# Kernel tuning notes

Hardware: AMD Instinct MI355X
Metric: run time of the kernel (lower is better)

The kernel has to match this reference:

```python
import jax, jax.numpy as jnp
import numpy as np

N_NODES_PER_GRAPH = 64
NUM_GRAPHS = 2048
N = NUM_GRAPHS * N_NODES_PER_GRAPH  # 131072 total nodes
E = N * 8                           # 1048576 edges
IN_DIM, H1, H2 = 64, 128, 64
OUT_DIM = (N_NODES_PER_GRAPH * N_NODES_PER_GRAPH - N_NODES_PER_GRAPH) // 2  # 2016


def setup_inputs() -> dict:
    key = jax.random.key(0)
    ks = jax.random.split(key, 16)
    s = 0.05
    x = jax.random.normal(ks[0], (N, IN_DIM), dtype=jnp.float32)
    # edges within each graph: offsets within graph + graph base offset
    src_local = jax.random.randint(ks[1], (E,), 0, N_NODES_PER_GRAPH)
    dst_local = jax.random.randint(ks[2], (E,), 0, N_NODES_PER_GRAPH)
    gid = jnp.repeat(jnp.arange(NUM_GRAPHS), E // NUM_GRAPHS) * N_NODES_PER_GRAPH
    edge_index = jnp.stack([src_local + gid, dst_local + gid]).astype(jnp.int64)
    batch = jnp.repeat(jnp.arange(NUM_GRAPHS), N_NODES_PER_GRAPH).astype(jnp.int64)
    eps = jax.random.normal(ks[3], (NUM_GRAPHS, H2), dtype=jnp.float32)
    return {
        "x": x, "edge_index": edge_index, "batch": batch, "eps": eps,
        "w1_rel": jax.random.normal(ks[4], (IN_DIM, H1)) * s,
        "b1": jnp.zeros((H1,), jnp.float32),
        "w1_root": jax.random.normal(ks[5], (IN_DIM, H1)) * s,
        "w2_rel": jax.random.normal(ks[6], (H1, H2)) * s,
        "b2": jnp.zeros((H2,), jnp.float32),
        "w2_root": jax.random.normal(ks[7], (H1, H2)) * s,
        "w3_rel": jax.random.normal(ks[8], (H1, H2)) * s,
        "b3": jnp.zeros((H2,), jnp.float32),
        "w3_root": jax.random.normal(ks[9], (H1, H2)) * s,
        "fc1_w": jax.random.normal(ks[10], (H2, H1)) * s,
        "fc1_b": jnp.zeros((H1,), jnp.float32),
        "fc2_w": jax.random.normal(ks[11], (H1, OUT_DIM)) * s,
        "fc2_b": jnp.zeros((OUT_DIM,), jnp.float32),
    }


def _graph_conv(h, src, dst, w_rel, b, w_root):
    # PyG GraphConv: out_i = W_rel @ (sum_{j in N(i)} h_j) + b + W_root @ h_i
    agg = jax.ops.segment_sum(h[src], dst, num_segments=N)  # [N, d_in]
    return agg @ w_rel + b + h @ w_root


def _segment_mean(h, seg):
    s = jax.ops.segment_sum(h, seg, num_segments=NUM_GRAPHS)
    cnt = jax.ops.segment_sum(jnp.ones((h.shape[0],), h.dtype), seg, num_segments=NUM_GRAPHS)
    return s / jnp.maximum(cnt, 1.0)[:, None]


def reference(x, edge_index, batch, eps, w1_rel, b1, w1_root, w2_rel, b2, w2_root,
              w3_rel, b3, w3_root, fc1_w, fc1_b, fc2_w, fc2_b):
    src, dst = edge_index[0], edge_index[1]
    # encode (dropout p=0.0 -> identity)
    h1 = jax.nn.relu(_graph_conv(x, src, dst, w1_rel, b1, w1_root))
    mu = _segment_mean(_graph_conv(h1, src, dst, w2_rel, b2, w2_root), batch)
    logvar = _segment_mean(_graph_conv(h1, src, dst, w3_rel, b3, w3_root), batch)
    # reparameterize with provided eps
    z = mu + eps * jnp.exp(0.5 * logvar)
    # decode
    h = jax.nn.relu(z @ fc1_w + fc1_b)
    recon = jax.nn.sigmoid(h @ fc2_w + fc2_b)
    return recon, mu, logvar
```

## Files before the change

### kernel.cpp

```cpp
#include <hip/hip_runtime.h>
#include <math.h>

#define NG 2048
#define NPG 64
#define EPG 512
#define ETOT (NG*EPG)
#define IND 64
#define H1D 128
#define H2D 64
#define OUTD 2016

typedef __attribute__((ext_vector_type(8))) short bf16x8;
typedef __attribute__((ext_vector_type(4))) float f32x4;
typedef __attribute__((ext_vector_type(8))) unsigned short u16x8;
typedef __attribute__((ext_vector_type(4))) short s16x4;

__device__ inline short f2b(float f) {
  union { float f; unsigned u; } v; v.f = f;
  unsigned r = (v.u + 0x7FFFu + ((v.u >> 16) & 1u)) >> 16;
  return (short)r;
}

__global__ void p_w1(const float* __restrict__ w1_rel, const float* __restrict__ w1_root,
                     short* __restrict__ WTgF,
                     const float* __restrict__ w2_rel, const float* __restrict__ w2_root,
                     const float* __restrict__ w3_rel, const float* __restrict__ w3_root,
                     const float* __restrict__ fc1_w,
                     short* __restrict__ W23T, short* __restrict__ fc1T) {
  __shared__ float L[4224];
  const int b = blockIdx.x;
  const int tid = threadIdx.x;
  if (b < 8) {
    const int ct = b;
    const int ks = tid >> 6, l = tid & 63;
    const int col = ct*16 + (l & 15);
    const int kb  = ks*32 + (l >> 4)*8;
    short tmp[8];
    #pragma unroll
    for (int j = 0; j < 8; ++j) {
      const int k = kb + j;
      float v = (k < 64) ? w1_rel[k*H1D + col] : w1_root[(k - 64)*H1D + col];
      tmp[j] = f2b(v);
    }
    *(uint4*)&WTgF[(size_t)((ct*4 + ks)*64 + l)*8] = *(uint4*)tmp;
  } else if (b < 12) {
    const int cc = b - 8;
    const int j0 = cc*32;
    const float* wrel  = (cc < 2) ? w2_rel  : w3_rel;
    const float* wroot = (cc < 2) ? w2_root : w3_root;
    const int jl = j0 & 63;
    const int c = tid >> 3, k0 = (tid & 7)*32;
    for (int i = tid; i < 4096; i += 256) {
      int k = i >> 5, cc2 = i & 31;
      L[k*33 + cc2] = wrel[k*H2D + jl + cc2];
    }
    __syncthreads();
    if (k0 < 128)
      for (int kk = 0; kk < 32; ++kk)
        W23T[(size_t)(j0 + c)*264 + k0 + kk] = f2b(L[(k0 + kk)*33 + c]);
    __syncthreads();
    for (int i = tid; i < 4096; i += 256) {
      int k = i >> 5, cc2 = i & 31;
      L[k*33 + cc2] = wroot[k*H2D + jl + cc2];
    }
    __syncthreads();
    if (k0 >= 128)
      for (int kk = 0; kk < 32; ++kk)
        W23T[(size_t)(j0 + c)*264 + k0 + kk] = f2b(L[(k0 + kk - 128)*33 + c]);
  } else {
    const int c0 = (b - 12)*64;
    for (int i = tid; i < 4096; i += 256) {
      int k = i >> 6, c = i & 63;
      L[k*65 + c] = fc1_w[k*H1D + c0 + c];
    }
    __syncthreads();
    const int c = tid >> 2, k0 = (tid & 3)*16;
    for (int kk = 0; kk < 16; ++kk)
      fc1T[(size_t)(c0 + c)*72 + k0 + kk] = f2b(L[(k0 + kk)*65 + c]);
  }
}

__global__ __launch_bounds__(256, 5) void k1_enc(
    const float* __restrict__ x, const int* __restrict__ ei,
    const short* __restrict__ WTgF, const float* __restrict__ b1,
    short* __restrict__ SVb,
    const float* __restrict__ fc2_w, short* __restrict__ WF2g)
{
  __shared__ __align__(16) char smem[31744];
  const int g = blockIdx.x;
  const int tid = threadIdx.x;

  if (g >= NG) {
    float* L = (float*)smem;
    const int bid = g - NG;
    const int c0 = bid*32;
    for (int i = tid; i < 4096; i += 256) {
      int k = i >> 5, c = i & 31;
      L[k*33 + c] = fc2_w[(size_t)k*OUTD + c0 + c];
    }
    __syncthreads();
    const int tl = tid >> 7;
    const int r  = tid & 127;
    const int ks = r >> 5;
    const int lp = r & 31;
    const int ct = bid*2 + tl;
    #pragma unroll
    for (int u = 0; u < 2; ++u) {
      const int l = lp*2 + u;
      const int cl = tl*16 + (l & 15);
      const int kb = ks*32 + (l >> 4)*8;
      short tmp[8];
      #pragma unroll
      for (int j = 0; j < 8; ++j) tmp[j] = f2b(L[(kb + j)*33 + cl]);
      *(uint4*)&WF2g[(size_t)((ct*4 + ks)*64 + l)*8] = *(uint4*)tmp;
    }
    return;
  }

  short* Xb   = (short*)smem;
  short* XbT  = (short*)(smem + 9216);
  short* Ab   = (short*)(smem + 18432);
  unsigned* Au32 = (unsigned*)(smem + 27648);

  const int w = tid >> 6, l = tid & 63;

  const int e0 = g*EPG + tid*2;
  const int2 sp = *(const int2*)&ei[e0];
  const int2 dp = *(const int2*)&ei[ETOT + e0];
  const int s0 = sp.x & 63, d0 = dp.x & 63;
  const int s1 = sp.y & 63, d1 = dp.y & 63;
  const int n = tid & 63, f0 = (tid >> 6) * 16;
  const float* xr = x + (size_t)g*(NPG*IND) + n*IND + f0;
  float4 v0 = *(const float4*)&xr[0];
  float4 v1 = *(const float4*)&xr[4];
  float4 v2 = *(const float4*)&xr[8];
  float4 v3 = *(const float4*)&xr[12];

  for (int i = tid; i < 64*16; i += 256) Au32[i] = 0u;
  __syncthreads();

  atomicAdd(&Au32[d0*16 + (s0 >> 2)], 1u << (8*(s0 & 3)));
  atomicAdd(&Au32[d1*16 + (s1 >> 2)], 1u << (8*(s1 & 3)));

  {
    u16x8 lo, hi;
    lo[0]=(unsigned short)f2b(v0.x); lo[1]=(unsigned short)f2b(v0.y);
    lo[2]=(unsigned short)f2b(v0.z); lo[3]=(unsigned short)f2b(v0.w);
    lo[4]=(unsigned short)f2b(v1.x); lo[5]=(unsigned short)f2b(v1.y);
    lo[6]=(unsigned short)f2b(v1.z); lo[7]=(unsigned short)f2b(v1.w);
    hi[0]=(unsigned short)f2b(v2.x); hi[1]=(unsigned short)f2b(v2.y);
    hi[2]=(unsigned short)f2b(v2.z); hi[3]=(unsigned short)f2b(v2.w);
    hi[4]=(unsigned short)f2b(v3.x); hi[5]=(unsigned short)f2b(v3.y);
    hi[6]=(unsigned short)f2b(v3.z); hi[7]=(unsigned short)f2b(v3.w);
    *(u16x8*)&Xb[n*72 + f0]     = lo;
    *(u16x8*)&Xb[n*72 + f0 + 8] = hi;
    #pragma unroll
    for (int j = 0; j < 8; ++j) {
      XbT[(f0 + j)*72 + n]     = (short)lo[j];
      XbT[(f0 + 8 + j)*72 + n] = (short)hi[j];
    }
  }
  __syncthreads();

  {
    const int row = tid >> 2, qw = tid & 3;
    unsigned wds[4];
    #pragma unroll
    for (int q = 0; q < 4; ++q) wds[q] = Au32[row*16 + qw*4 + q];
    auto pk = [](unsigned wv, int p) -> unsigned {
      unsigned c0 = (wv >> (16*p)) & 255u, c1 = (wv >> (16*p + 8)) & 255u;
      return (unsigned)(unsigned short)f2b((float)c0)
           | ((unsigned)(unsigned short)f2b((float)c1) << 16);
    };
    uint4 oA = { pk(wds[0],0), pk(wds[0],1), pk(wds[1],0), pk(wds[1],1) };
    uint4 oB = { pk(wds[2],0), pk(wds[2],1), pk(wds[3],0), pk(wds[3],1) };
    unsigned* abp = (unsigned*)&Ab[row*72 + qw*16];
    *(uint4*)&abp[0] = oA;
    *(uint4*)&abp[4] = oB;
  }

  {
    const int squad = tid >> 4;
    const int db = (tid & 15) * 4;
    unsigned ps = 0;
    #pragma unroll
    for (int i = 0; i < 4; ++i) ps += Au32[(db + i)*16 + squad];
    ps += __shfl_xor(ps, 1); ps += __shfl_xor(ps, 2);
    ps += __shfl_xor(ps, 4); ps += __shfl_xor(ps, 8);
    if ((tid & 15) == 0) {
      #pragma unroll
      for (int i = 0; i < 4; ++i)
        *(float*)&Ab[(squad*4 + i)*72 + 64] = (float)((ps >> (8*i)) & 255u);
    }
  }

  const int rm = w*16;
  const int fr = l & 15;
  const int koff = (l >> 4) * 8;

  f32x4 agc[4];
  #pragma unroll
  for (int t = 0; t < 4; ++t) agc[t] = (f32x4){0.f,0.f,0.f,0.f};
  #pragma unroll
  for (int ks = 0; ks < 2; ++ks) {
    bf16x8 badj = *(const bf16x8*)&Ab[(rm + fr)*72 + ks*32 + koff];
    #pragma unroll
    for (int t = 0; t < 4; ++t) {
      bf16x8 axt = *(const bf16x8*)&XbT[(t*16 + fr)*72 + ks*32 + koff];
      agc[t] = __builtin_amdgcn_mfma_f32_16x16x32_bf16(axt, badj, agc[t], 0, 0, 0);
    }
  }

  bf16x8 bfr[2][4];
  #pragma unroll
  for (int ct2 = 0; ct2 < 2; ++ct2)
    #pragma unroll
    for (int ks = 0; ks < 4; ++ks)
      bfr[ct2][ks] = *(const bf16x8*)&WTgF[(size_t)(((2*w + ct2)*4 + ks)*64 + l)*8];

  short* AGb = Ab;
  #pragma unroll
  for (int t = 0; t < 4; ++t) {
    s16x4 vv;
    #pragma unroll
    for (int r = 0; r < 4; ++r) vv[r] = f2b(agc[t][r]);
    *(s16x4*)&AGb[(rm + (l & 15))*72 + t*16 + (l >> 4)*4] = vv;
  }

  __syncthreads();

  const float bb0 = b1[(2*w)*16 + fr];
  const float bb1 = b1[(2*w + 1)*16 + fr];
  float hs0 = 0.f, ws0 = 0.f, hs1 = 0.f, ws1 = 0.f;
  #pragma unroll
  for (int rt = 0; rt < 4; ++rt) {
    bf16x8 afr[4];
    #pragma unroll
    for (int ks = 0; ks < 4; ++ks)
      afr[ks] = (ks < 2)
        ? *(const bf16x8*)&AGb[(rt*16 + fr)*72 + ks*32 + koff]
        : *(const bf16x8*)&Xb[(rt*16 + fr)*72 + (ks - 2)*32 + koff];
    f32x4 a0 = (f32x4){0.f,0.f,0.f,0.f}, a1 = (f32x4){0.f,0.f,0.f,0.f};
    #pragma unroll
    for (int ks = 0; ks < 4; ++ks) {
      a0 = __builtin_amdgcn_mfma_f32_16x16x32_bf16(afr[ks], bfr[0][ks], a0, 0, 0, 0);
      a1 = __builtin_amdgcn_mfma_f32_16x16x32_bf16(afr[ks], bfr[1][ks], a1, 0, 0, 0);
    }
    #pragma unroll
    for (int r = 0; r < 4; ++r) {
      const float dgr = *(const float*)&Ab[(rt*16 + (l>>4)*4 + r)*72 + 64];
      float va = fmaxf(a0[r] + bb0, 0.f);
      float vb = fmaxf(a1[r] + bb1, 0.f);
      hs0 += va; ws0 += dgr*va;
      hs1 += vb; ws1 += dgr*vb;
    }
  }
  hs0 += __shfl_down(hs0, 32); ws0 += __shfl_down(ws0, 32);
  hs1 += __shfl_down(hs1, 32); ws1 += __shfl_down(ws1, 32);
  hs0 += __shfl_down(hs0, 16); ws0 += __shfl_down(ws0, 16);
  hs1 += __shfl_down(hs1, 16); ws1 += __shfl_down(ws1, 16);
  if (l < 16) {
    short* svg = SVb + (size_t)g*256;
    svg[(2*w)*16 + l]           = f2b(ws0);
    svg[(2*w + 1)*16 + l]       = f2b(ws1);
    svg[128 + (2*w)*16 + l]     = f2b(hs0);
    svg[128 + (2*w + 1)*16 + l] = f2b(hs1);
  }
}

__global__ __launch_bounds__(256) void k1b_latent(
    const short* __restrict__ SVb, const short* __restrict__ W23T,
    const float* __restrict__ b2, const float* __restrict__ b3,
    const float* __restrict__ eps, const short* __restrict__ fc1T,
    const float* __restrict__ fc1_b,
    float* __restrict__ out_mu, float* __restrict__ out_lv, short* __restrict__ hbufF)
{
  __shared__ short SV[32*264];
  __shared__ short Zt[32*72];
  const int g0 = blockIdx.x * 32;
  const int tid = threadIdx.x;
  const int w = tid >> 6, l = tid & 63;
  const int s = w >> 1;
  const int h = w & 1;
  const int fr = l & 15;
  const int koff = (l >> 4) * 8;

  for (int i = tid; i < 32*64; i += 256) {
    const int r = i >> 6, kq = (i & 63)*4;
    *(s16x4*)&SV[r*264 + kq] = *(const s16x4*)&SVb[(size_t)(g0 + r)*256 + kq];
  }
  __syncthreads();

  f32x4 acc[4];
  #pragma unroll
  for (int t = 0; t < 4; ++t) acc[t] = (f32x4){0.f,0.f,0.f,0.f};
  #pragma unroll
  for (int ks = 0; ks < 8; ++ks) {
    bf16x8 a = *(const bf16x8*)&SV[(s*16 + fr)*264 + ks*32 + koff];
    #pragma unroll
    for (int j = 0; j < 2; ++j) {
      bf16x8 bm = *(const bf16x8*)&W23T[((2*h + j)*16 + fr)*264 + ks*32 + koff];
      bf16x8 bl = *(const bf16x8*)&W23T[((2*h + j + 4)*16 + fr)*264 + ks*32 + koff];
      acc[j]     = __builtin_amdgcn_mfma_f32_16x16x32_bf16(bm, a, acc[j], 0, 0, 0);
      acc[2 + j] = __builtin_amdgcn_mfma_f32_16x16x32_bf16(bl, a, acc[2 + j], 0, 0, 0);
    }
  }
  {
    const int grow = s*16 + (l & 15);
    const size_t gg = (size_t)(g0 + grow);
    #pragma unroll
    for (int j = 0; j < 2; ++j) {
      const int c0 = (2*h + j)*16 + (l >> 4)*4;
      const float4 bb2 = *(const float4*)&b2[c0];
      const float4 bb3 = *(const float4*)&b3[c0];
      const float4 ev  = *(const float4*)&eps[gg*64 + c0];
      float4 mu, lv;
      mu.x = acc[j][0]*(1.f/64.f) + bb2.x;  lv.x = acc[2+j][0]*(1.f/64.f) + bb3.x;
      mu.y = acc[j][1]*(1.f/64.f) + bb2.y;  lv.y = acc[2+j][1]*(1.f/64.f) + bb3.y;
      mu.z = acc[j][2]*(1.f/64.f) + bb2.z;  lv.z = acc[2+j][2]*(1.f/64.f) + bb3.z;
      mu.w = acc[j][3]*(1.f/64.f) + bb2.w;  lv.w = acc[2+j][3]*(1.f/64.f) + bb3.w;
      *(float4*)&out_mu[gg*64 + c0] = mu;
      *(float4*)&out_lv[gg*64 + c0] = lv;
      s16x4 zs;
      zs[0] = f2b(mu.x + ev.x * __expf(0.5f*lv.x));
      zs[1] = f2b(mu.y + ev.y * __expf(0.5f*lv.y));
      zs[2] = f2b(mu.z + ev.z * __expf(0.5f*lv.z));
      zs[3] = f2b(mu.w + ev.w * __expf(0.5f*lv.w));
      *(s16x4*)&Zt[grow*72 + c0] = zs;
    }
  }
  __syncthreads();

  f32x4 hacc[4];
  #pragma unroll
  for (int t = 0; t < 4; ++t) hacc[t] = (f32x4){0.f,0.f,0.f,0.f};
  #pragma unroll
  for (int ks = 0; ks < 2; ++ks) {
    bf16x8 a = *(const bf16x8*)&Zt[(s*16 + fr)*72 + ks*32 + koff];
    #pragma unroll
    for (int j = 0; j < 4; ++j) {
      bf16x8 b = *(const bf16x8*)&fc1T[((h*4 + j)*16 + fr)*72 + ks*32 + koff];
      hacc[j] = __builtin_amdgcn_mfma_f32_16x16x32_bf16(b, a, hacc[j], 0, 0, 0);
    }
  }
  {
    const int row = s*16 + (l & 15);
    const int rt2 = blockIdx.x*2 + (row >> 4);
    #pragma unroll
    for (int j = 0; j < 4; ++j) {
      const int c0 = (h*4 + j)*16 + (l >> 4)*4;
      const float4 bb = *(const float4*)&fc1_b[c0];
      s16x4 hv;
      hv[0] = f2b(fmaxf(hacc[j][0] + bb.x, 0.f));
      hv[1] = f2b(fmaxf(hacc[j][1] + bb.y, 0.f));
      hv[2] = f2b(fmaxf(hacc[j][2] + bb.z, 0.f));
      hv[3] = f2b(fmaxf(hacc[j][3] + bb.w, 0.f));
      const int ks2 = c0 >> 5;
      const int q   = (c0 >> 3) & 3;
      const int j8  = c0 & 7;
      const int lane = (row & 15) + 16*q;
      *(s16x4*)&hbufF[(size_t)((rt2*4 + ks2)*64 + lane)*8 + j8] = hv;
    }
  }
}

__global__ __launch_bounds__(256, 8) void k2_decoder(
    const short* __restrict__ hbufF, const short* __restrict__ WF2g,
    const float* __restrict__ fc2_b, float* __restrict__ recon)
{
  const int bx = blockIdx.x, by = blockIdx.y;
  const int tid = threadIdx.x;
  const int w = tid >> 6, l = tid & 63;
  const int rt = bx*4 + w;

  bf16x8 ah[4];
  #pragma unroll
  for (int ks = 0; ks < 4; ++ks)
    ah[ks] = *(const bf16x8*)&hbufF[(size_t)((rt*4 + ks)*64 + l)*8];

  f32x4 acc[6];
  #pragma unroll
  for (int t = 0; t < 6; ++t) acc[t] = (f32x4){0.f,0.f,0.f,0.f};

  #pragma unroll
  for (int ks = 0; ks < 4; ++ks) {
    #pragma unroll
    for (int t = 0; t < 6; ++t) {
      const int ct = by*6 + t;
      bf16x8 bw = *(const bf16x8*)&WF2g[(size_t)((ct*4 + ks)*64 + l)*8];
      acc[t] = __builtin_amdgcn_mfma_f32_16x16x32_bf16(bw, ah[ks], acc[t], 0, 0, 0);
    }
  }

  const int row = bx*64 + w*16 + (l & 15);
  #pragma unroll
  for (int t = 0; t < 6; ++t) {
    const int colq = (by*6 + t)*16 + (l >> 4)*4;
    const float4 bb = *(const float4*)&fc2_b[colq];
    float4 o;
    o.x = 1.f/(1.f + __expf(-(acc[t][0] + bb.x)));
    o.y = 1.f/(1.f + __expf(-(acc[t][1] + bb.y)));
    o.z = 1.f/(1.f + __expf(-(acc[t][2] + bb.z)));
    o.w = 1.f/(1.f + __expf(-(acc[t][3] + bb.w)));
    *(float4*)&recon[(size_t)row*OUTD + colq] = o;
  }
}

extern "C" void kernel_launch(void* const* d_in, const int* in_sizes, int n_in,
                              void* d_out, int out_size, void* d_ws, size_t ws_size,
                              hipStream_t stream) {
  const float* x       = (const float*)d_in[0];
  const int*   ei      = (const int*)d_in[1];
  const float* eps     = (const float*)d_in[3];
  const float* w1_rel  = (const float*)d_in[4];
  const float* b1      = (const float*)d_in[5];
  const float* w1_root = (const float*)d_in[6];
  const float* w2_rel  = (const float*)d_in[7];
  const float* b2      = (const float*)d_in[8];
  const float* w2_root = (const float*)d_in[9];
  const float* w3_rel  = (const float*)d_in[10];
  const float* b3      = (const float*)d_in[11];
  const float* w3_root = (const float*)d_in[12];
  const float* fc1_w   = (const float*)d_in[13];
  const float* fc1_b   = (const float*)d_in[14];
  const float* fc2_w   = (const float*)d_in[15];
  const float* fc2_b   = (const float*)d_in[16];

  float* recon  = (float*)d_out;
  float* out_mu = recon + (size_t)NG*OUTD;
  float* out_lv = out_mu + (size_t)NG*H2D;

  char* p = (char*)d_ws;
  short* WTgF  = (short*)p;              p += 8*4*64*8*2;
  short* WF2g  = (short*)p;              p += 126*4*64*8*2;
  short* fc1T  = (short*)p;              p += 128*72*2;
  short* W23T  = (short*)p;              p += 128*264*2;
  short* SVb   = (short*)p;              p += (size_t)NG*256*2;
  short* hbufF = (short*)p;

  p_w1<<<14, 256, 0, stream>>>(w1_rel, w1_root, WTgF,
                               w2_rel, w2_root, w3_rel, w3_root,
                               fc1_w, W23T, fc1T);
  k1_enc<<<NG + 63, 256, 0, stream>>>(x, ei, WTgF, b1, SVb, fc2_w, WF2g);
  k1b_latent<<<64, 256, 0, stream>>>(SVb, W23T, b2, b3, eps, fc1T, fc1_b,
                                     out_mu, out_lv, hbufF);
  k2_decoder<<<dim3(32, 21), 256, 0, stream>>>(hbufF, WF2g, fc2_b, recon);
}
```

Baseline: 136.9 us.

## Fuse encoder, latent and decoder into one cooperative persistent kernel

Merges the encoder, latent and decoder kernels into a single cooperative kernel of 1024 blocks. Each block encodes two graphs, then grid-wide syncs separate the latent and decoder phases, so per-kernel launch gaps and tail effects go away. The fc2 weight repacking moves into the prep kernel, and decode work is split into half-width units so 1344 of them spread over the persistent grid. In exchange, grid syncs add cost, occupancy is capped at 4 blocks per CU, and the latent phase runs on only 64 blocks while the rest wait; separate fallback kernels are kept in case the cooperative launch is not possible.

```diff
diff --git a/kernel.cpp b/kernel.cpp
--- a/kernel.cpp
+++ b/kernel.cpp
@@ -1,4 +1,5 @@
 #include <hip/hip_runtime.h>
+#include <hip/hip_cooperative_groups.h>
 #include <math.h>
 
 #define NG 2048
@@ -26,7 +27,8 @@
                      const float* __restrict__ w2_rel, const float* __restrict__ w2_root,
                      const float* __restrict__ w3_rel, const float* __restrict__ w3_root,
                      const float* __restrict__ fc1_w,
-                     short* __restrict__ W23T, short* __restrict__ fc1T) {
+                     short* __restrict__ W23T, short* __restrict__ fc1T,
+                     const float* __restrict__ fc2_w, short* __restrict__ WF2g) {
   __shared__ float L[4224];
   const int b = blockIdx.x;
   const int tid = threadIdx.x;
@@ -67,7 +69,7 @@
     if (k0 >= 128)
       for (int kk = 0; kk < 32; ++kk)
         W23T[(size_t)(j0 + c)*264 + k0 + kk] = f2b(L[(k0 + kk - 128)*33 + c]);
-  } else {
+  } else if (b < 14) {
     const int c0 = (b - 12)*64;
     for (int i = tid; i < 4096; i += 256) {
       int k = i >> 6, c = i & 63;
@@ -77,22 +79,8 @@
     const int c = tid >> 2, k0 = (tid & 3)*16;
     for (int kk = 0; kk < 16; ++kk)
       fc1T[(size_t)(c0 + c)*72 + k0 + kk] = f2b(L[(k0 + kk)*65 + c]);
-  }
-}
-
-__global__ __launch_bounds__(256, 5) void k1_enc(
-    const float* __restrict__ x, const int* __restrict__ ei,
-    const short* __restrict__ WTgF, const float* __restrict__ b1,
-    short* __restrict__ SVb,
-    const float* __restrict__ fc2_w, short* __restrict__ WF2g)
-{
-  __shared__ __align__(16) char smem[31744];
-  const int g = blockIdx.x;
-  const int tid = threadIdx.x;
-
-  if (g >= NG) {
-    float* L = (float*)smem;
-    const int bid = g - NG;
+  } else {
+    const int bid = b - 14;
     const int c0 = bid*32;
     for (int i = tid; i < 4096; i += 256) {
       int k = i >> 5, c = i & 31;
@@ -114,22 +102,31 @@
       for (int j = 0; j < 8; ++j) tmp[j] = f2b(L[(kb + j)*33 + cl]);
       *(uint4*)&WF2g[(size_t)((ct*4 + ks)*64 + l)*8] = *(uint4*)tmp;
     }
-    return;
-  }
-
+  }
+}
+
+__device__ __forceinline__ void enc_graph(
+    int g, int tid, char* smem,
+    const float* __restrict__ x, const int* __restrict__ ei,
+    const bf16x8 (&bfr)[2][4], float bb0, float bb1,
+    short* __restrict__ SVb)
+{
   short* Xb   = (short*)smem;
   short* XbT  = (short*)(smem + 9216);
   short* Ab   = (short*)(smem + 18432);
   unsigned* Au32 = (unsigned*)(smem + 27648);
 
   const int w = tid >> 6, l = tid & 63;
+  const int fr = l & 15;
+  const int koff = (l >> 4) * 8;
+  const int rm = w*16;
+  const int n = tid & 63, f0 = (tid >> 6) * 16;
 
   const int e0 = g*EPG + tid*2;
   const int2 sp = *(const int2*)&ei[e0];
   const int2 dp = *(const int2*)&ei[ETOT + e0];
   const int s0 = sp.x & 63, d0 = dp.x & 63;
   const int s1 = sp.y & 63, d1 = dp.y & 63;
-  const int n = tid & 63, f0 = (tid >> 6) * 16;
   const float* xr = x + (size_t)g*(NPG*IND) + n*IND + f0;
   float4 v0 = *(const float4*)&xr[0];
   float4 v1 = *(const float4*)&xr[4];
@@ -194,10 +191,6 @@
     }
   }
 
-  const int rm = w*16;
-  const int fr = l & 15;
-  const int koff = (l >> 4) * 8;
-
   f32x4 agc[4];
   #pragma unroll
   for (int t = 0; t < 4; ++t) agc[t] = (f32x4){0.f,0.f,0.f,0.f};
@@ -210,27 +203,15 @@
       agc[t] = __builtin_amdgcn_mfma_f32_16x16x32_bf16(axt, badj, agc[t], 0, 0, 0);
     }
   }
-
-  bf16x8 bfr[2][4];
-  #pragma unroll
-  for (int ct2 = 0; ct2 < 2; ++ct2)
-    #pragma unroll
-    for (int ks = 0; ks < 4; ++ks)
-      bfr[ct2][ks] = *(const bf16x8*)&WTgF[(size_t)(((2*w + ct2)*4 + ks)*64 + l)*8];
-
-  short* AGb = Ab;
   #pragma unroll
   for (int t = 0; t < 4; ++t) {
     s16x4 vv;
     #pragma unroll
     for (int r = 0; r < 4; ++r) vv[r] = f2b(agc[t][r]);
-    *(s16x4*)&AGb[(rm + (l & 15))*72 + t*16 + (l >> 4)*4] = vv;
-  }
-
+    *(s16x4*)&Ab[(rm + (l & 15))*72 + t*16 + (l >> 4)*4] = vv;
+  }
   __syncthreads();
 
-  const float bb0 = b1[(2*w)*16 + fr];
-  const float bb1 = b1[(2*w + 1)*16 + fr];
   float hs0 = 0.f, ws0 = 0.f, hs1 = 0.f, ws1 = 0.f;
   #pragma unroll
   for (int rt = 0; rt < 4; ++rt) {
@@ -238,7 +219,7 @@
     #pragma unroll
     for (int ks = 0; ks < 4; ++ks)
       afr[ks] = (ks < 2)
-        ? *(const bf16x8*)&AGb[(rt*16 + fr)*72 + ks*32 + koff]
+        ? *(const bf16x8*)&Ab[(rt*16 + fr)*72 + ks*32 + koff]
         : *(const bf16x8*)&Xb[(rt*16 + fr)*72 + (ks - 2)*32 + koff];
     f32x4 a0 = (f32x4){0.f,0.f,0.f,0.f}, a1 = (f32x4){0.f,0.f,0.f,0.f};
     #pragma unroll
@@ -268,17 +249,17 @@
   }
 }
 
-__global__ __launch_bounds__(256) void k1b_latent(
+__device__ __forceinline__ void latent_group(
+    int g0, int tid, char* smem,
     const short* __restrict__ SVb, const short* __restrict__ W23T,
     const float* __restrict__ b2, const float* __restrict__ b3,
     const float* __restrict__ eps, const short* __restrict__ fc1T,
     const float* __restrict__ fc1_b,
-    float* __restrict__ out_mu, float* __restrict__ out_lv, short* __restrict__ hbufF)
-{
-  __shared__ short SV[32*264];
-  __shared__ short Zt[32*72];
-  const int g0 = blockIdx.x * 32;
-  const int tid = threadIdx.x;
+    float* __restrict__ out_mu, float* __restrict__ out_lv,
+    short* __restrict__ hbufF)
+{
+  short* SV = (short*)smem;
+  short* Zt = (short*)(smem + 16896);
   const int w = tid >> 6, l = tid & 63;
   const int s = w >> 1;
   const int h = w & 1;
@@ -345,7 +326,7 @@
   }
   {
     const int row = s*16 + (l & 15);
-    const int rt2 = blockIdx.x*2 + (row >> 4);
+    const int rt2 = (g0 >> 4) + (row >> 4);
     #pragma unroll
     for (int j = 0; j < 4; ++j) {
       const int c0 = (h*4 + j)*16 + (l >> 4)*4;
@@ -364,38 +345,39 @@
   }
 }
 
-__global__ __launch_bounds__(256, 8) void k2_decoder(
+__device__ __forceinline__ void decode32(
+    int u, int tid,
     const short* __restrict__ hbufF, const short* __restrict__ WF2g,
     const float* __restrict__ fc2_b, float* __restrict__ recon)
 {
-  const int bx = blockIdx.x, by = blockIdx.y;
-  const int tid = threadIdx.x;
   const int w = tid >> 6, l = tid & 63;
-  const int rt = bx*4 + w;
+  const int rowblk = u & 63;
+  const int cb = u >> 6;
+  const int rt = rowblk*2 + (w >> 1);
+  const int h2 = w & 1;
 
   bf16x8 ah[4];
   #pragma unroll
   for (int ks = 0; ks < 4; ++ks)
     ah[ks] = *(const bf16x8*)&hbufF[(size_t)((rt*4 + ks)*64 + l)*8];
 
-  f32x4 acc[6];
-  #pragma unroll
-  for (int t = 0; t < 6; ++t) acc[t] = (f32x4){0.f,0.f,0.f,0.f};
-
+  f32x4 acc[3];
+  #pragma unroll
+  for (int t = 0; t < 3; ++t) acc[t] = (f32x4){0.f,0.f,0.f,0.f};
   #pragma unroll
   for (int ks = 0; ks < 4; ++ks) {
     #pragma unroll
-    for (int t = 0; t < 6; ++t) {
-      const int ct = by*6 + t;
+    for (int t = 0; t < 3; ++t) {
+      const int ct = cb*6 + h2*3 + t;
       bf16x8 bw = *(const bf16x8*)&WF2g[(size_t)((ct*4 + ks)*64 + l)*8];
       acc[t] = __builtin_amdgcn_mfma_f32_16x16x32_bf16(bw, ah[ks], acc[t], 0, 0, 0);
     }
   }
 
-  const int row = bx*64 + w*16 + (l & 15);
-  #pragma unroll
-  for (int t = 0; t < 6; ++t) {
-    const int colq = (by*6 + t)*16 + (l >> 4)*4;
+  const int row = rt*16 + (l & 15);
+  #pragma unroll
+  for (int t = 0; t < 3; ++t) {
+    const int colq = (cb*6 + h2*3 + t)*16 + (l >> 4)*4;
     const float4 bb = *(const float4*)&fc2_b[colq];
     float4 o;
     o.x = 1.f/(1.f + __expf(-(acc[t][0] + bb.x)));
@@ -404,6 +386,86 @@
     o.w = 1.f/(1.f + __expf(-(acc[t][3] + bb.w)));
     *(float4*)&recon[(size_t)row*OUTD + colq] = o;
   }
+}
+
+__global__ __launch_bounds__(256, 4) void mega(
+    const float* __restrict__ x, const int* __restrict__ ei,
+    const short* __restrict__ WTgF, const float* __restrict__ b1,
+    short* __restrict__ SVb, const short* __restrict__ W23T,
+    const float* __restrict__ b2, const float* __restrict__ b3,
+    const float* __restrict__ eps, const short* __restrict__ fc1T,
+    const float* __restrict__ fc1_b,
+    float* __restrict__ out_mu, float* __restrict__ out_lv,
+    short* __restrict__ hbufF, const short* __restrict__ WF2g,
+    const float* __restrict__ fc2_b, float* __restrict__ recon)
+{
+  __shared__ __align__(16) char smem[31744];
+  const int bid = blockIdx.x;
+  const int tid = threadIdx.x;
+  const int w = tid >> 6, l = tid & 63;
+  const int fr = l & 15;
+
+  bf16x8 bfr[2][4];
+  #pragma unroll
+  for (int ct2 = 0; ct2 < 2; ++ct2)
+    #pragma unroll
+    for (int ks = 0; ks < 4; ++ks)
+      bfr[ct2][ks] = *(const bf16x8*)&WTgF[(size_t)(((2*w + ct2)*4 + ks)*64 + l)*8];
+  const float bb0 = b1[(2*w)*16 + fr];
+  const float bb1 = b1[(2*w + 1)*16 + fr];
+
+  enc_graph(2*bid,     tid, smem, x, ei, bfr, bb0, bb1, SVb);
+  enc_graph(2*bid + 1, tid, smem, x, ei, bfr, bb0, bb1, SVb);
+
+  cooperative_groups::this_grid().sync();
+
+  if (bid < 64)
+    latent_group(bid*32, tid, smem, SVb, W23T, b2, b3, eps, fc1T, fc1_b,
+                 out_mu, out_lv, hbufF);
+
+  cooperative_groups::this_grid().sync();
+
+  for (int u = 1023 - bid; u < 1344; u += 1024)
+    decode32(u, tid, hbufF, WF2g, fc2_b, recon);
+}
+
+__global__ __launch_bounds__(256, 5) void k1_fb(
+    const float* __restrict__ x, const int* __restrict__ ei,
+    const short* __restrict__ WTgF, const float* __restrict__ b1,
+    short* __restrict__ SVb)
+{
+  __shared__ __align__(16) char smem[31744];
+  const int tid = threadIdx.x;
+  const int w = tid >> 6, l = tid & 63;
+  const int fr = l & 15;
+  bf16x8 bfr[2][4];
+  #pragma unroll
+  for (int ct2 = 0; ct2 < 2; ++ct2)
+    #pragma unroll
+    for (int ks = 0; ks < 4; ++ks)
+      bfr[ct2][ks] = *(const bf16x8*)&WTgF[(size_t)(((2*w + ct2)*4 + ks)*64 + l)*8];
+  const float bb0 = b1[(2*w)*16 + fr];
+  const float bb1 = b1[(2*w + 1)*16 + fr];
+  enc_graph(blockIdx.x, tid, smem, x, ei, bfr, bb0, bb1, SVb);
+}
+
+__global__ __launch_bounds__(256) void k1b_fb(
+    const short* __restrict__ SVb, const short* __restrict__ W23T,
+    const float* __restrict__ b2, const float* __restrict__ b3,
+    const float* __restrict__ eps, const short* __restrict__ fc1T,
+    const float* __restrict__ fc1_b,
+    float* __restrict__ out_mu, float* __restrict__ out_lv, short* __restrict__ hbufF)
+{
+  __shared__ __align__(16) char smem[21504];
+  latent_group(blockIdx.x*32, threadIdx.x, smem, SVb, W23T, b2, b3, eps,
+               fc1T, fc1_b, out_mu, out_lv, hbufF);
+}
+
+__global__ __launch_bounds__(256, 8) void k2_fb(
+    const short* __restrict__ hbufF, const short* __restrict__ WF2g,
+    const float* __restrict__ fc2_b, float* __restrict__ recon)
+{
+  decode32((blockIdx.y << 6) | blockIdx.x, threadIdx.x, hbufF, WF2g, fc2_b, recon);
 }
 
 extern "C" void kernel_launch(void* const* d_in, const int* in_sizes, int n_in,
@@ -438,11 +500,24 @@
   short* SVb   = (short*)p;              p += (size_t)NG*256*2;
   short* hbufF = (short*)p;
 
-  p_w1<<<14, 256, 0, stream>>>(w1_rel, w1_root, WTgF,
+  p_w1<<<77, 256, 0, stream>>>(w1_rel, w1_root, WTgF,
                                w2_rel, w2_root, w3_rel, w3_root,
-                               fc1_w, W23T, fc1T);
-  k1_enc<<<NG + 63, 256, 0, stream>>>(x, ei, WTgF, b1, SVb, fc2_w, WF2g);
-  k1b_latent<<<64, 256, 0, stream>>>(SVb, W23T, b2, b3, eps, fc1T, fc1_b,
-                                     out_mu, out_lv, hbufF);
-  k2_decoder<<<dim3(32, 21), 256, 0, stream>>>(hbufF, WF2g, fc2_b, recon);
-}
+                               fc1_w, W23T, fc1T, fc2_w, WF2g);
+
+  int nb = 0;
+  hipError_t oe = hipOccupancyMaxActiveBlocksPerMultiprocessor(&nb, mega, 256, 0);
+  if (oe == hipSuccess && nb >= 4) {
+    void* args[17] = {
+      (void*)&x, (void*)&ei, (void*)&WTgF, (void*)&b1, (void*)&SVb,
+      (void*)&W23T, (void*)&b2, (void*)&b3, (void*)&eps, (void*)&fc1T,
+      (void*)&fc1_b, (void*)&out_mu, (void*)&out_lv, (void*)&hbufF,
+      (void*)&WF2g, (void*)&fc2_b, (void*)&recon };
+    hipLaunchCooperativeKernel((const void*)mega, dim3(1024), dim3(256),
+                               args, 0, stream);
+  } else {
+    k1_fb<<<NG, 256, 0, stream>>>(x, ei, WTgF, b1, SVb);
+    k1b_fb<<<64, 256, 0, stream>>>(SVb, W23T, b2, b3, eps, fc1T, fc1_b,
+                                   out_mu, out_lv, hbufF);
+    k2_fb<<<dim3(64, 21), 256, 0, stream>>>(hbufF, WF2g, fc2_b, recon);
+  }
+}
```

Measured after the change: 142.9 us. 1.04x slower.
